# Performance work log

Measured on AMD Instinct MI355X. Metric: run time of the kernel, lower is better.

Reference implementation:

```python
import math
import jax, jax.numpy as jnp
import numpy as np

H = 8      # num_heads
K = 3      # polynomial order
WH, WW = 8, 8  # win_size


def _relative_position_index(wh, ww):
    coords = np.stack(np.meshgrid(np.arange(wh), np.arange(ww), indexing='ij'))  # [2,wh,ww]
    cf = coords.reshape(2, -1)                       # [2, N]
    rel = cf[:, :, None] - cf[:, None, :]            # [2, N, N]
    rel = rel.transpose(1, 2, 0).astype(np.int64)    # [N, N, 2]
    rel[..., 0] += wh - 1
    rel[..., 1] += ww - 1
    rel[..., 0] *= 2 * ww - 1
    return rel.sum(-1)                               # [N, N]


def setup_inputs() -> dict:
    key = jax.random.key(0)
    ks = jax.random.split(key, 10)
    B, N, C = 1024, WH * WW, 256
    hd = C // H
    s = 0.02
    inp = {
        'x': jax.random.normal(ks[0], (B, N, C), dtype=jnp.float32),
        'Wq': jax.random.normal(ks[1], (C, C), dtype=jnp.float32) * s,
        'bq': jnp.zeros((C,), dtype=jnp.float32),
        'Wkv': jax.random.normal(ks[2], (C, 2 * C), dtype=jnp.float32) * s,
        'bkv': jnp.zeros((2 * C,), dtype=jnp.float32),
        'Wgate': jax.random.normal(ks[3], (hd, K + 1), dtype=jnp.float32) * s,
        'bgate': jnp.zeros((K + 1,), dtype=jnp.float32),
        'Wproj': jax.random.normal(ks[4], (C, C), dtype=jnp.float32) * s,
        'bproj': jnp.zeros((C,), dtype=jnp.float32),
        'bias_table': jax.random.normal(ks[5], ((2 * WH - 1) * (2 * WW - 1), H), dtype=jnp.float32) * s,
        'rel_index': jnp.asarray(_relative_position_index(WH, WW)),
    }
    return inp


def reference(x, Wq, bq, Wkv, bkv, Wgate, bgate, Wproj, bproj, bias_table, rel_index):
    B, N, C = x.shape
    hd = C // H
    # per-(batch,head) sigmoid gates over the K+1 polynomial orders
    gate = jax.nn.sigmoid(x.mean(axis=1).reshape(B, H, hd) @ Wgate + bgate)  # [B,H,K+1]
    gate = gate[..., None, None]                                             # [B,H,K+1,1,1]

    q = (x @ Wq + bq).reshape(B, N, H, hd).transpose(0, 2, 1, 3)             # [B,H,N,hd]
    kv = (x @ Wkv + bkv).reshape(B, N, 2, H, hd).transpose(2, 0, 3, 1, 4)
    k, v = kv[0], kv[1]                                                      # [B,H,N,hd]

    q = jax.nn.softmax(q, axis=-1)
    k = jax.nn.softmax(k, axis=-1)
    attn = jnp.einsum('bhnd,bhmd->bhnm', q, k)                               # [B,H,N,N] (>=0)

    bias = bias_table[rel_index.reshape(-1)].reshape(N, N, H).transpose(2, 0, 1)  # [H,N,N]
    attn = attn + jax.nn.relu(bias)[None]
    attn = (attn + attn.transpose(0, 1, 3, 2)) * 0.5

    # symmetric degree normalization: D^{-1/2} A D^{-1/2}, zero-degree rows untouched
    d = attn.sum(axis=-1)                                                    # [B,H,N]
    dn = jnp.where(d > 0, 1.0 / jnp.sqrt(jnp.where(d > 0, d, 1.0)), d)
    attn = attn * dn[:, :, None, :] * dn[:, :, :, None]

    I = jnp.eye(N, dtype=attn.dtype)
    L = I - attn        # Laplacian
    L_hat = I + attn    # 2I - L

    # tmp[i] = L_hat^i (tmp[0] = I broadcasts)
    tmp = [I]
    E = I
    for _ in range(K):
        E = E @ L_hat
        tmp.append(E)

    c = [math.comb(K, j) / 2 ** K for j in range(K + 1)]
    out = c[0] * gate[:, :, K] * (tmp[K] @ v)                                # [B,H,N,hd]
    E = I
    for j in range(K):
        E = E @ L
        out = out + c[j + 1] * gate[:, :, j] * (E @ (tmp[K - j - 1] @ v))

    out = out.transpose(0, 2, 1, 3).reshape(B, N, C)
    out = out @ Wproj + bproj
    return out
```

## Files before the change

kernel.cpp:

```cpp
#include <hip/hip_runtime.h>
#include <hip/hip_bf16.h>

typedef __attribute__((ext_vector_type(8))) short bf16x8;
typedef __attribute__((ext_vector_type(4))) float f32x4;

__device__ __forceinline__ unsigned short f2bf(float f) {
    union { __hip_bfloat16 h; unsigned short u; } c;
    c.h = __float2bfloat16(f);
    return c.u;
}
__device__ __forceinline__ unsigned int pk2(float lo, float hi) {
    return (unsigned int)f2bf(lo) | ((unsigned int)f2bf(hi) << 16);
}
__device__ __forceinline__ bf16x8 as_bf(uint4 u) {
    union { uint4 a; bf16x8 b; } c; c.a = u; return c.b;
}
__device__ __forceinline__ float bf2f(unsigned short us) {
    return __uint_as_float(((unsigned int)us) << 16);
}
__device__ __forceinline__ void gload_lds16(const void* g, void* l) {
    __builtin_amdgcn_global_load_lds(
        (const __attribute__((address_space(1))) void*)g,
        (__attribute__((address_space(3))) void*)l, 16, 0, 0);
}

__global__ __launch_bounds__(256) void prep_kernel(
    const float* __restrict__ x,
    const float* __restrict__ Wq, const float* __restrict__ Wkv, const float* __restrict__ Wproj,
    const float* __restrict__ Wgate, const float* __restrict__ bgate,
    const float* __restrict__ bias_table, const int* __restrict__ rel_index,
    unsigned short* __restrict__ xbf, int use_xbf,
    unsigned short* __restrict__ wq, unsigned short* __restrict__ wk,
    unsigned short* __restrict__ wv, unsigned short* __restrict__ wp,
    float* __restrict__ bsym, float* __restrict__ wpoly)
{
    const int bid = blockIdx.x, t = threadIdx.x;
    if (bid < 1024) {
        __shared__ float mean_s[256];
        __shared__ float gsig[32];
        const float* xb = x + (size_t)bid * 16384;
        float s = 0.f;
        if (use_xbf) {
            unsigned short* xo = xbf + (size_t)bid * 16384;
            #pragma unroll 4
            for (int n = 0; n < 64; n++) { float v = xb[n * 256 + t]; s += v; xo[n * 256 + t] = f2bf(v); }
        } else {
            #pragma unroll 8
            for (int n = 0; n < 64; n++) s += xb[n * 256 + t];
        }
        mean_s[t] = s * (1.f / 64.f);
        __syncthreads();
        if (t < 32) {
            int h = t >> 2, j = t & 3;
            float g = bgate[j];
            #pragma unroll 8
            for (int dd = 0; dd < 32; dd++) g = fmaf(mean_s[h * 32 + dd], Wgate[dd * 4 + j], g);
            gsig[t] = 1.f / (1.f + __expf(-g));
        }
        __syncthreads();
        if (t < 8) {
            float g0 = gsig[t * 4], g1 = gsig[t * 4 + 1], g2 = gsig[t * 4 + 2], g3 = gsig[t * 4 + 3];
            float a = 0.125f * g3, bb = 0.375f * g0, cc = 0.375f * g1, dd = 0.125f * g2;
            float4 o;
            o.x = a + bb + cc + dd;
            o.y = 3.f * a + bb - cc - 3.f * dd;
            o.z = 3.f * a - bb - cc + 3.f * dd;
            o.w = a - bb + cc - dd;
            ((float4*)wpoly)[bid * 8 + t] = o;
        }
    } else if (bid < 2048) {
        int e = (bid - 1024) * 256 + t;
        int m = e >> 16, r = e & 65535, o = r >> 8, kk = r & 255;
        float v; unsigned short* dst;
        if (m == 0)      { v = Wq[kk * 256 + o];        dst = wq; }
        else if (m == 1) { v = Wkv[kk * 512 + o];       dst = wk; }
        else if (m == 2) { v = Wkv[kk * 512 + 256 + o]; dst = wv; }
        else             { v = Wproj[kk * 256 + o];     dst = wp; }
        dst[o * 256 + kk] = f2bf(v);
    } else {
        int e = (bid - 2048) * 256 + t;
        int hh = e >> 12, ij = e & 4095;
        int i = ij >> 6, j = ij & 63;
        float bij = bias_table[rel_index[ij] * 8 + hh];
        float bji = bias_table[rel_index[j * 64 + i] * 8 + hh];
        bsym[hh * 4096 + ij] = 0.5f * (fmaxf(bij, 0.f) + fmaxf(bji, 0.f));
    }
}

template <bool XBF>
__global__ __launch_bounds__(256, 4) void attn_kernel(
    const float* __restrict__ x, const unsigned short* __restrict__ xbf,
    const float* __restrict__ bq, const float* __restrict__ bkv,
    const unsigned short* __restrict__ wq, const unsigned short* __restrict__ wk,
    const unsigned short* __restrict__ wv,
    const float* __restrict__ bsym, const float* __restrict__ wpoly,
    unsigned short* __restrict__ hid)
{
    __shared__ __align__(16) unsigned char tile[32768];
    float* dn = (float*)(tile + 28672);

    const int bid = blockIdx.x;
    const int xcd = bid & 7, idx = bid >> 3;
    const int b = xcd * 128 + (idx >> 3), h = idx & 7;
    const int t = threadIdx.x;
    const int l = t & 63, w = t >> 6;
    const int lr = l & 15, qg = l >> 4;

    const float4 wv4 = ((const float4*)wpoly)[b * 8 + h];

    const int role = w;
    uint4 Bfr0[8], Bfr1[8];
    {
        const unsigned short* wsel = (role == 0) ? wq : (role == 1) ? wk : wv;
        const uint4* Wp = (const uint4*)wsel;
        const int ct0 = (role < 2) ? 0 : (role - 2);
        const int o0 = h * 32 + ct0 * 16 + lr;
        #pragma unroll
        for (int ks = 0; ks < 8; ks++) Bfr0[ks] = Wp[o0 * 32 + ks * 4 + qg];
        if (role < 2) {
            #pragma unroll
            for (int ks = 0; ks < 8; ks++) Bfr1[ks] = Wp[(o0 + 16) * 32 + ks * 4 + qg];
        }
    }

    if (XBF) {
        const unsigned short* xb = xbf + (size_t)b * 16384;
        const int rp = l >> 5, u = l & 31;
        #pragma unroll
        for (int i = 0; i < 8; i++) {
            int row = i * 8 + w * 2 + rp;
            int csrc = (u & 24) | ((u & 7) ^ (row & 7));
            gload_lds16(xb + row * 256 + csrc * 8, tile + (i * 8 + w * 2) * 512);
        }
    } else {
        const float* xb = x + (size_t)b * 16384;
        #pragma unroll
        for (int i = 0; i < 8; i++) {
            int e = t + i * 256;
            int row = e >> 5, c = e & 31;
            const float4* p = (const float4*)(xb + row * 256 + c * 8);
            float4 f0 = p[0], f1 = p[1];
            uint4 u;
            u.x = pk2(f0.x, f0.y); u.y = pk2(f0.z, f0.w);
            u.z = pk2(f1.x, f1.y); u.w = pk2(f1.z, f1.w);
            *(uint4*)(tile + row * 512 + ((c >> 3) << 7) + (((c & 7) ^ (row & 7)) << 4)) = u;
        }
    }

    f32x4 acc0[4], acc1[4];
    {
        const int ct0 = (role < 2) ? 0 : (role - 2);
        const int o0 = h * 32 + ct0 * 16 + lr;
        float b0 = (role == 0) ? bq[o0] : (role == 1) ? bkv[o0] : bkv[256 + o0];
        float b1 = (role == 0) ? bq[o0 + 16] : (role == 1) ? bkv[o0 + 16] : 0.f;
        #pragma unroll
        for (int mt = 0; mt < 4; mt++) {
            f32x4 z0 = {b0, b0, b0, b0}; acc0[mt] = z0;
            f32x4 z1 = {b1, b1, b1, b1}; acc1[mt] = z1;
        }
    }
    __syncthreads();

    if (role < 2) {
        #pragma unroll
        for (int mt = 0; mt < 4; mt++) {
            const int rowA = mt * 16 + lr;
            #pragma unroll
            for (int ks = 0; ks < 8; ks++) {
                const int c = ks * 4 + qg;
                bf16x8 af = *(const bf16x8*)(tile + rowA * 512 + ((c >> 3) << 7) + (((c & 7) ^ (rowA & 7)) << 4));
                acc0[mt] = __builtin_amdgcn_mfma_f32_16x16x32_bf16(af, as_bf(Bfr0[ks]), acc0[mt], 0, 0, 0);
                acc1[mt] = __builtin_amdgcn_mfma_f32_16x16x32_bf16(af, as_bf(Bfr1[ks]), acc1[mt], 0, 0, 0);
            }
        }
    } else {
        #pragma unroll
        for (int mt = 0; mt < 4; mt++) {
            const int rowA = mt * 16 + lr;
            #pragma unroll
            for (int ks = 0; ks < 8; ks++) {
                const int c = ks * 4 + qg;
                bf16x8 af = *(const bf16x8*)(tile + rowA * 512 + ((c >> 3) << 7) + (((c & 7) ^ (rowA & 7)) << 4));
                acc0[mt] = __builtin_amdgcn_mfma_f32_16x16x32_bf16(af, as_bf(Bfr0[ks]), acc0[mt], 0, 0, 0);
            }
        }
    }
    __syncthreads();

    float bsv[4][4];
    {
        const float* bh_ = bsym + h * 4096;
        #pragma unroll
        for (int jt = 0; jt < 4; jt++)
            #pragma unroll
            for (int r = 0; r < 4; r++)
                bsv[jt][r] = bh_[(w * 16 + qg * 4 + r) * 64 + jt * 16 + lr];
    }

    if (role < 2) {
        #pragma unroll
        for (int mt = 0; mt < 4; mt++)
            #pragma unroll
            for (int r = 0; r < 4; r++) {
                float e0 = __expf(acc0[mt][r]), e1 = __expf(acc1[mt][r]);
                float s = e0 + e1;
                s += __shfl_xor(s, 1); s += __shfl_xor(s, 2);
                s += __shfl_xor(s, 4); s += __shfl_xor(s, 8);
                float inv = 1.f / s;
                acc0[mt][r] = e0 * inv; acc1[mt][r] = e1 * inv;
            }
    }

    if (role == 0) {
        #pragma unroll
        for (int mt = 0; mt < 4; mt++)
            #pragma unroll
            for (int r = 0; r < 4; r++) {
                int row = mt * 16 + qg * 4 + r;
                int d0 = lr, d1 = 16 + lr;
                *(short*)(tile + row * 128 + (((d0 >> 3) ^ (row & 7)) << 4) + (d0 & 7) * 2) = (short)f2bf(acc0[mt][r]);
                *(short*)(tile + row * 128 + (((d1 >> 3) ^ (row & 7)) << 4) + (d1 & 7) * 2) = (short)f2bf(acc1[mt][r]);
            }
    } else if (role == 1) {
        #pragma unroll
        for (int mt = 0; mt < 4; mt++)
            #pragma unroll
            for (int r = 0; r < 4; r++) {
                int row = mt * 16 + qg * 4 + r;
                int d0 = lr, d1 = 16 + lr;
                *(short*)(tile + 8192 + row * 128 + (((d0 >> 3) ^ (row & 7)) << 4) + (d0 & 7) * 2) = (short)f2bf(acc0[mt][r]);
                *(short*)(tile + 8192 + row * 128 + (((d1 >> 3) ^ (row & 7)) << 4) + (d1 & 7) * 2) = (short)f2bf(acc1[mt][r]);
            }
    } else {
        const int d = (role - 2) * 16 + lr;
        #pragma unroll
        for (int mt = 0; mt < 4; mt++)
            #pragma unroll
            for (int r = 0; r < 4; r++) {
                int row = mt * 16 + qg * 4 + r;
                *(short*)(tile + 16384 + d * 128 + (((row >> 3) ^ (d & 7)) << 4) + (row & 7) * 2) = (short)f2bf(acc0[mt][r]);
            }
    }
    __syncthreads();

    float sv[4][4];
    float dnv[4];
    {
        const int swz = (qg ^ (lr & 7)) << 4;
        bf16x8 aqf = *(const bf16x8*)(tile + (w * 16 + lr) * 128 + swz);
        bf16x8 akf = *(const bf16x8*)(tile + 8192 + (w * 16 + lr) * 128 + swz);
        float rs[4] = {0.f, 0.f, 0.f, 0.f};
        #pragma unroll
        for (int jt = 0; jt < 4; jt++) {
            bf16x8 bqf = *(const bf16x8*)(tile + (jt * 16 + lr) * 128 + swz);
            bf16x8 bkf = *(const bf16x8*)(tile + 8192 + (jt * 16 + lr) * 128 + swz);
            f32x4 qk = {0.f, 0.f, 0.f, 0.f}, kq = {0.f, 0.f, 0.f, 0.f};
            qk = __builtin_amdgcn_mfma_f32_16x16x32_bf16(aqf, bkf, qk, 0, 0, 0);
            kq = __builtin_amdgcn_mfma_f32_16x16x32_bf16(akf, bqf, kq, 0, 0, 0);
            #pragma unroll
            for (int r = 0; r < 4; r++) {
                float v = 0.5f * (qk[r] + kq[r]) + bsv[jt][r];
                sv[jt][r] = v;
                rs[r] += v;
            }
        }
        #pragma unroll
        for (int r = 0; r < 4; r++) {
            float s = rs[r];
            s += __shfl_xor(s, 1); s += __shfl_xor(s, 2);
            s += __shfl_xor(s, 4); s += __shfl_xor(s, 8);
            dnv[r] = (s > 0.f) ? rsqrtf(s) : s;
        }
        if (lr == 0) {
            int base = w * 16 + qg * 4;
            dn[base + 0] = dnv[0]; dn[base + 1] = dnv[1];
            dn[base + 2] = dnv[2]; dn[base + 3] = dnv[3];
        }
    }
    __syncthreads();

    {
        float dnj[4];
        #pragma unroll
        for (int jt = 0; jt < 4; jt++) dnj[jt] = dn[jt * 16 + lr];
        #pragma unroll
        for (int jt = 0; jt < 4; jt++)
            #pragma unroll
            for (int r = 0; r < 4; r++) {
                int i = w * 16 + qg * 4 + r, j = jt * 16 + lr;
                *(short*)(tile + i * 128 + (((j >> 3) ^ (i & 7)) << 4) + (j & 7) * 2)
                    = (short)f2bf(sv[jt][r] * dnv[r] * dnj[jt]);
            }
    }
    __syncthreads();

    const float w0c = wv4.x, w1c = wv4.y, w2c = wv4.z, w3c = wv4.w;
    f32x4 y[2];
    #pragma unroll
    for (int ct = 0; ct < 2; ct++)
        #pragma unroll
        for (int r = 0; r < 4; r++) {
            int row = w * 16 + qg * 4 + r;
            int d = ct * 16 + lr;
            unsigned short us = *(unsigned short*)(tile + 16384 + d * 128 + (((row >> 3) ^ (d & 7)) << 4) + (row & 7) * 2);
            y[ct][r] = w0c * bf2f(us);
        }

#define AU_ROUND(SRC, DST, WC, WRITE) {                                                          \
    f32x4 u0 = {0.f,0.f,0.f,0.f}, u1 = {0.f,0.f,0.f,0.f};                                        \
    _Pragma("unroll")                                                                            \
    for (int ks2 = 0; ks2 < 2; ks2++) {                                                          \
        int c = ks2 * 4 + qg;                                                                    \
        bf16x8 af = *(const bf16x8*)(tile + (w * 16 + lr) * 128 + ((c ^ (lr & 7)) << 4));        \
        bf16x8 b0 = *(const bf16x8*)(tile + (SRC) + lr * 128 + ((c ^ (lr & 7)) << 4));           \
        bf16x8 b1 = *(const bf16x8*)(tile + (SRC) + (16 + lr) * 128 + ((c ^ (lr & 7)) << 4));    \
        u0 = __builtin_amdgcn_mfma_f32_16x16x32_bf16(af, b0, u0, 0, 0, 0);                       \
        u1 = __builtin_amdgcn_mfma_f32_16x16x32_bf16(af, b1, u1, 0, 0, 0);                       \
    }                                                                                            \
    y[0] += (WC) * u0; y[1] += (WC) * u1;                                                        \
    if (WRITE) {                                                                                 \
        _Pragma("unroll")                                                                        \
        for (int r = 0; r < 4; r++) {                                                            \
            int i = w * 16 + qg * 4 + r;                                                         \
            *(short*)(tile + (DST) + lr * 128 + (((i >> 3) ^ (lr & 7)) << 4) + (i & 7) * 2) = (short)f2bf(u0[r]); \
            *(short*)(tile + (DST) + (16 + lr) * 128 + (((i >> 3) ^ (lr & 7)) << 4) + (i & 7) * 2) = (short)f2bf(u1[r]); \
        }                                                                                        \
    }                                                                                            \
    __syncthreads();                                                                             \
}
    AU_ROUND(16384, 20480, w1c, 1)
    AU_ROUND(20480, 24576, w2c, 1)
    AU_ROUND(24576, 0,     w3c, 0)
#undef AU_ROUND

    #pragma unroll
    for (int ct = 0; ct < 2; ct++)
        #pragma unroll
        for (int r = 0; r < 4; r++) {
            int row = w * 16 + qg * 4 + r;
            int col = h * 32 + ct * 16 + lr;
            hid[((size_t)b * 64 + row) * 256 + col] = f2bf(y[ct][r]);
        }
}

__global__ __launch_bounds__(256) void proj_kernel(
    const unsigned short* __restrict__ hidden,
    const unsigned short* __restrict__ wp,
    const float* __restrict__ bproj,
    float* __restrict__ out)
{
    __shared__ __align__(16) unsigned char atile[65536];
    const int rb = blockIdx.x;
    const int t = threadIdx.x, l = t & 63, w = t >> 6;
    const int lr = l & 15, qg = l >> 4;

    const unsigned short* hb = hidden + (size_t)rb * 128 * 256;
    {
        const int rp = l >> 5, u = l & 31;
        #pragma unroll
        for (int i = 0; i < 16; i++) {
            int row = i * 8 + w * 2 + rp;
            int csrc = (u & 24) | ((u & 7) ^ (row & 7));
            gload_lds16(hb + row * 256 + csrc * 8, atile + (i * 8 + w * 2) * 512);
        }
    }
    float bzv[16];
    #pragma unroll
    for (int ct = 0; ct < 16; ct++) bzv[ct] = bproj[ct * 16 + lr];
    __syncthreads();

    bf16x8 af[2][8];
    #pragma unroll
    for (int rt = 0; rt < 2; rt++) {
        int row = w * 32 + rt * 16 + lr;
        #pragma unroll
        for (int ks = 0; ks < 8; ks++) {
            int c = ks * 4 + qg;
            af[rt][ks] = *(const bf16x8*)(atile + row * 512 + (((c & 24) | ((c & 7) ^ (row & 7))) << 4));
        }
    }

    const uint4* WP = (const uint4*)wp;
    #pragma unroll 2
    for (int ct = 0; ct < 16; ct++) {
        f32x4 a0 = {0.f, 0.f, 0.f, 0.f}, a1 = {0.f, 0.f, 0.f, 0.f};
        #pragma unroll
        for (int ks = 0; ks < 8; ks++) {
            bf16x8 bf = as_bf(WP[(ct * 16 + lr) * 32 + ks * 4 + qg]);
            a0 = __builtin_amdgcn_mfma_f32_16x16x32_bf16(af[0][ks], bf, a0, 0, 0, 0);
            a1 = __builtin_amdgcn_mfma_f32_16x16x32_bf16(af[1][ks], bf, a1, 0, 0, 0);
        }
        int colg = ct * 16 + lr;
        float bz = bzv[ct];
        #pragma unroll
        for (int r = 0; r < 4; r++) {
            int rowg = rb * 128 + w * 32 + qg * 4 + r;
            out[(size_t)rowg * 256 + colg] = a0[r] + bz;
            out[(size_t)(rowg + 16) * 256 + colg] = a1[r] + bz;
        }
    }
}

extern "C" void kernel_launch(void* const* d_in, const int* in_sizes, int n_in,
                              void* d_out, int out_size, void* d_ws, size_t ws_size,
                              hipStream_t stream) {
    const float* x          = (const float*)d_in[0];
    const float* Wq         = (const float*)d_in[1];
    const float* bq         = (const float*)d_in[2];
    const float* Wkv        = (const float*)d_in[3];
    const float* bkv        = (const float*)d_in[4];
    const float* Wgate      = (const float*)d_in[5];
    const float* bgate      = (const float*)d_in[6];
    const float* Wproj      = (const float*)d_in[7];
    const float* bproj      = (const float*)d_in[8];
    const float* bias_table = (const float*)d_in[9];
    const int*   rel_index  = (const int*)d_in[10];
    float* out = (float*)d_out;
    unsigned char* wsb = (unsigned char*)d_ws;

    const size_t HID   = 0;
    const size_t WQo   = 33554432;
    const size_t WKo   = WQo + 131072;
    const size_t WVo   = WKo + 131072;
    const size_t WPo   = WVo + 131072;
    const size_t BIASo = WPo + 131072;
    const size_t WPOLY = BIASo + 131072;
    const size_t XBFo  = WPOLY + 131072;
    const int use_xbf  = (ws_size >= XBFo + 33554432ull) ? 1 : 0;

    unsigned short* hid = (unsigned short*)(wsb + HID);
    unsigned short* wq  = (unsigned short*)(wsb + WQo);
    unsigned short* wk  = (unsigned short*)(wsb + WKo);
    unsigned short* wv  = (unsigned short*)(wsb + WVo);
    unsigned short* wp  = (unsigned short*)(wsb + WPo);
    float* bsym  = (float*)(wsb + BIASo);
    float* wpoly = (float*)(wsb + WPOLY);
    unsigned short* xbf = (unsigned short*)(wsb + XBFo);

    prep_kernel<<<dim3(2176), dim3(256), 0, stream>>>(
        x, Wq, Wkv, Wproj, Wgate, bgate, bias_table, rel_index,
        xbf, use_xbf, wq, wk, wv, wp, bsym, wpoly);
    if (use_xbf)
        attn_kernel<true><<<dim3(8192), dim3(256), 0, stream>>>(
            x, xbf, bq, bkv, wq, wk, wv, bsym, wpoly, hid);
    else
        attn_kernel<false><<<dim3(8192), dim3(256), 0, stream>>>(
            x, xbf, bq, bkv, wq, wk, wv, bsym, wpoly, hid);
    proj_kernel<<<dim3(512), dim3(256), 0, stream>>>(hid, wp, bproj, out);
}
```

Before: 142.5 us.

## Shrink attention LDS footprint via double-buffered K-chunk staging of x

The 64x256 x tile is no longer staged whole into LDS (32KB). It is now loaded in four 64-column chunks into two 8KB ping-pong buffers, and the next chunk is staged while MFMA runs on the current one. LDS drops to about 20KB, the launch-bounds occupancy hint rises from 4 to 7 blocks, and the later buffer offsets are remapped. In exchange there are more barriers, and the higher occupancy hint may force register spills given the large per-thread weight fragments.

```diff
diff --git a/kernel.cpp b/kernel.cpp
--- a/kernel.cpp
+++ b/kernel.cpp
@@ -88,7 +88,7 @@
 }
 
 template <bool XBF>
-__global__ __launch_bounds__(256, 4) void attn_kernel(
+__global__ __launch_bounds__(256, 7) void attn_kernel(
     const float* __restrict__ x, const unsigned short* __restrict__ xbf,
     const float* __restrict__ bq, const float* __restrict__ bkv,
     const unsigned short* __restrict__ wq, const unsigned short* __restrict__ wk,
@@ -96,8 +96,8 @@
     const float* __restrict__ bsym, const float* __restrict__ wpoly,
     unsigned short* __restrict__ hid)
 {
-    __shared__ __align__(16) unsigned char tile[32768];
-    float* dn = (float*)(tile + 28672);
+    __shared__ __align__(16) unsigned char tile[20736];
+    float* dn = (float*)(tile + 20480);
 
     const int bid = blockIdx.x;
     const int xcd = bid & 7, idx = bid >> 3;
@@ -123,30 +123,6 @@
         }
     }
 
-    if (XBF) {
-        const unsigned short* xb = xbf + (size_t)b * 16384;
-        const int rp = l >> 5, u = l & 31;
-        #pragma unroll
-        for (int i = 0; i < 8; i++) {
-            int row = i * 8 + w * 2 + rp;
-            int csrc = (u & 24) | ((u & 7) ^ (row & 7));
-            gload_lds16(xb + row * 256 + csrc * 8, tile + (i * 8 + w * 2) * 512);
-        }
-    } else {
-        const float* xb = x + (size_t)b * 16384;
-        #pragma unroll
-        for (int i = 0; i < 8; i++) {
-            int e = t + i * 256;
-            int row = e >> 5, c = e & 31;
-            const float4* p = (const float4*)(xb + row * 256 + c * 8);
-            float4 f0 = p[0], f1 = p[1];
-            uint4 u;
-            u.x = pk2(f0.x, f0.y); u.y = pk2(f0.z, f0.w);
-            u.z = pk2(f1.x, f1.y); u.w = pk2(f1.z, f1.w);
-            *(uint4*)(tile + row * 512 + ((c >> 3) << 7) + (((c & 7) ^ (row & 7)) << 4)) = u;
-        }
-    }
-
     f32x4 acc0[4], acc1[4];
     {
         const int ct0 = (role < 2) ? 0 : (role - 2);
@@ -159,33 +135,65 @@
             f32x4 z1 = {b1, b1, b1, b1}; acc1[mt] = z1;
         }
     }
-    __syncthreads();
-
-    if (role < 2) {
-        #pragma unroll
-        for (int mt = 0; mt < 4; mt++) {
-            const int rowA = mt * 16 + lr;
-            #pragma unroll
-            for (int ks = 0; ks < 8; ks++) {
-                const int c = ks * 4 + qg;
-                bf16x8 af = *(const bf16x8*)(tile + rowA * 512 + ((c >> 3) << 7) + (((c & 7) ^ (rowA & 7)) << 4));
-                acc0[mt] = __builtin_amdgcn_mfma_f32_16x16x32_bf16(af, as_bf(Bfr0[ks]), acc0[mt], 0, 0, 0);
-                acc1[mt] = __builtin_amdgcn_mfma_f32_16x16x32_bf16(af, as_bf(Bfr1[ks]), acc1[mt], 0, 0, 0);
-            }
-        }
-    } else {
-        #pragma unroll
-        for (int mt = 0; mt < 4; mt++) {
-            const int rowA = mt * 16 + lr;
-            #pragma unroll
-            for (int ks = 0; ks < 8; ks++) {
-                const int c = ks * 4 + qg;
-                bf16x8 af = *(const bf16x8*)(tile + rowA * 512 + ((c >> 3) << 7) + (((c & 7) ^ (rowA & 7)) << 4));
-                acc0[mt] = __builtin_amdgcn_mfma_f32_16x16x32_bf16(af, as_bf(Bfr0[ks]), acc0[mt], 0, 0, 0);
-            }
-        }
-    }
-    __syncthreads();
+
+    const unsigned short* xbb = XBF ? (xbf + (size_t)b * 16384) : (unsigned short*)0;
+    const float* xbf32 = XBF ? (const float*)0 : (x + (size_t)b * 16384);
+
+#define STAGE_Q(QK, BUF) {                                                                   \
+    if (XBF) {                                                                               \
+        _Pragma("unroll")                                                                    \
+        for (int i = 0; i < 2; i++) {                                                        \
+            int rbase = w * 16 + i * 8;                                                      \
+            int row = rbase + (l >> 3);                                                      \
+            int u = l & 7;                                                                   \
+            int csrc = u ^ (row & 7);                                                        \
+            gload_lds16(xbb + row * 256 + (QK) * 64 + csrc * 8,                              \
+                        tile + (BUF) * 8192 + rbase * 128);                                  \
+        }                                                                                    \
+    } else {                                                                                 \
+        _Pragma("unroll")                                                                    \
+        for (int i = 0; i < 2; i++) {                                                        \
+            int e = t + i * 256;                                                             \
+            int row = e >> 3, u = e & 7;                                                     \
+            const float4* p = (const float4*)(xbf32 + row * 256 + (QK) * 64 + u * 8);        \
+            float4 f0 = p[0], f1 = p[1];                                                     \
+            uint4 uu;                                                                        \
+            uu.x = pk2(f0.x, f0.y); uu.y = pk2(f0.z, f0.w);                                  \
+            uu.z = pk2(f1.x, f1.y); uu.w = pk2(f1.z, f1.w);                                  \
+            *(uint4*)(tile + (BUF) * 8192 + row * 128 + ((u ^ (row & 7)) << 4)) = uu;        \
+        }                                                                                    \
+    }                                                                                        \
+}
+
+#define COMPUTE_Q(QK, BUF) {                                                                 \
+    _Pragma("unroll")                                                                        \
+    for (int mt = 0; mt < 4; mt++) {                                                         \
+        const int rowA = mt * 16 + lr;                                                       \
+        _Pragma("unroll")                                                                    \
+        for (int ks2 = 0; ks2 < 2; ks2++) {                                                  \
+            const int c = ks2 * 4 + qg;                                                      \
+            bf16x8 af = *(const bf16x8*)(tile + (BUF) * 8192 + rowA * 128 + ((c ^ (rowA & 7)) << 4)); \
+            acc0[mt] = __builtin_amdgcn_mfma_f32_16x16x32_bf16(af, as_bf(Bfr0[(QK) * 2 + ks2]), acc0[mt], 0, 0, 0); \
+            if (role < 2)                                                                    \
+                acc1[mt] = __builtin_amdgcn_mfma_f32_16x16x32_bf16(af, as_bf(Bfr1[(QK) * 2 + ks2]), acc1[mt], 0, 0, 0); \
+        }                                                                                    \
+    }                                                                                        \
+}
+
+    STAGE_Q(0, 0)
+    __syncthreads();
+    STAGE_Q(1, 1)
+    COMPUTE_Q(0, 0)
+    __syncthreads();
+    STAGE_Q(2, 0)
+    COMPUTE_Q(1, 1)
+    __syncthreads();
+    STAGE_Q(3, 1)
+    COMPUTE_Q(2, 0)
+    __syncthreads();
+    COMPUTE_Q(3, 1)
+#undef STAGE_Q
+#undef COMPUTE_Q
 
     float bsv[4][4];
     {
@@ -210,6 +218,7 @@
                 acc0[mt][r] = e0 * inv; acc1[mt][r] = e1 * inv;
             }
     }
+    __syncthreads();
 
     if (role == 0) {
         #pragma unroll
@@ -328,9 +337,9 @@
     }                                                                                            \
     __syncthreads();                                                                             \
 }
-    AU_ROUND(16384, 20480, w1c, 1)
-    AU_ROUND(20480, 24576, w2c, 1)
-    AU_ROUND(24576, 0,     w3c, 0)
+    AU_ROUND(16384, 8192,  w1c, 1)
+    AU_ROUND(8192,  12288, w2c, 1)
+    AU_ROUND(12288, 0,     w3c, 0)
 #undef AU_ROUND
 
     #pragma unroll
```

After: 278.8 us. 1.96x slower.
